# Kernel optimization log

Measured on AMD Instinct MI355X. Metric: run time of the kernel, lower is better.

The kernel has to match this reference:

```python
import jax, jax.numpy as jnp
import numpy as np

B, N, C_IN, C_OUT = 2, 163842, 64, 64  # icosphere level-7 vertex count
K = 7  # 1-ring neighborhood size (center + 6 neighbors)


def setup_inputs() -> dict:
    key = jax.random.key(0)
    kx, kw, kb, kn = jax.random.split(key, 4)
    x = jax.random.normal(kx, (B, N, C_IN), dtype=jnp.float32)
    # nn.Linear(7*in_feats, out_feats): W is (out, 7*in), bias (out,)
    W = jax.random.normal(kw, (C_OUT, K * C_IN), dtype=jnp.float32) * (1.0 / np.sqrt(K * C_IN))
    b = jax.random.normal(kb, (C_OUT,), dtype=jnp.float32) * 0.01
    neigh_orders = jax.random.randint(kn, (K * N,), 0, N, dtype=jnp.int64)
    return {"x": x, "W": W, "b": b, "neigh_orders": neigh_orders}


def reference(x, W, b, neigh_orders):
    # Faithful translation of onering_conv_layer_batch.forward:
    #   x: (B, N, C) -> permute -> (B, C, N)
    #   gather 7N indices on vertex axis -> (B, C, 7N)
    #   view -> (B, N, 7C)  (raw reshape of the (C, 7N) block, as in the torch code)
    #   Linear(7C -> out)
    Bb, Nn, Cc = x.shape
    xp = jnp.transpose(x, (0, 2, 1))            # (B, C, N)
    g = jnp.take(xp, neigh_orders, axis=2)      # (B, C, 7N)
    mat = g.reshape(Bb, Nn, K * Cc)             # (B, N, 7C)
    return jnp.einsum('bnk,ok->bno', mat, W) + b
```

## Files before the change

### kernel.cpp

```cpp
#include <hip/hip_runtime.h>

typedef short bf8_t __attribute__((ext_vector_type(8)));
typedef float f32x4 __attribute__((ext_vector_type(4)));

static constexpr int Bc      = 2;
static constexpr int Nv      = 163842;
static constexpr int CIN     = 64;
static constexpr int COUT    = 64;
static constexpr int KK      = 448;
static constexpr int SEVEN_N = 7 * Nv;
static constexpr int Q       = 3;
static constexpr int LM      = Q * KK;
static constexpr int MSTAGE  = LM + KK;
static constexpr int STRIDE  = 1800;
static constexpr int NT      = (SEVEN_N + LM - 1) / LM;
static constexpr int THREADS = 512;

__device__ inline unsigned pack2_bf16(float a, float b) {
    unsigned ua = __builtin_bit_cast(unsigned, a);
    unsigned ub = __builtin_bit_cast(unsigned, b);
    ua = (ua + 0x7FFFu + ((ua >> 16) & 1u)) >> 16;
    ub = (ub + 0x7FFFu + ((ub >> 16) & 1u));
    return (ua & 0xFFFFu) | (ub & 0xFFFF0000u);
}

__global__ __launch_bounds__(256) void xconv(const float* __restrict__ x,
                                             short* __restrict__ xb, int n) {
    const int i = (blockIdx.x * 256 + threadIdx.x) * 8;
    if (i >= n) return;
    const float4 a = *(const float4*)(x + i);
    const float4 c = *(const float4*)(x + i + 4);
    uint4 o;
    o.x = pack2_bf16(a.x, a.y); o.y = pack2_bf16(a.z, a.w);
    o.z = pack2_bf16(c.x, c.y); o.w = pack2_bf16(c.z, c.w);
    *(uint4*)(xb + i) = o;
}

__global__ __launch_bounds__(THREADS, 4) void conv_main_bf16(
    const short* __restrict__ xbf,
    const short* __restrict__ Wb,
    const float* __restrict__ bias,
    const int*   __restrict__ idx,
    float*       __restrict__ out)
{
    __shared__ short tile[16 * STRIDE];

    const int bid   = blockIdx.x;
    const int s     = bid & 7;
    const int b     = s & 1;
    const int mtres = s >> 1;
    const int rr    = bid >> 3;
    const int mt    = (rr >> 2) * 4 + mtres;
    const int cg    = rr & 3;
    if (mt >= NT) return;

    const int t    = threadIdx.x;
    const int M0   = mt * LM;
    const int mEnd = min(M0 + MSTAGE, SEVEN_N);
    const short* xb = xbf + (size_t)b * Nv * CIN;

    const int q     = t & 1;
    const int mloc  = t >> 1;
    const int choff = cg * 16 + q * 8;

    int iv[7];
    #pragma unroll
    for (int p = 0; p < 7; ++p) {
        const int m = M0 + p * 256 + mloc;
        iv[p] = (m < mEnd) ? idx[m] : 0;
    }
    bf8_t v[7];
    #pragma unroll
    for (int p = 0; p < 7; ++p)
        v[p] = *(const bf8_t*)(xb + (size_t)iv[p] * CIN + choff);
    #pragma unroll
    for (int p = 0; p < 7; ++p) {
        const int m = M0 + p * 256 + mloc;
        if (m < mEnd) {
            const int dm = m - M0;
            #pragma unroll
            for (int j = 0; j < 8; ++j) {
                const int c     = q * 8 + j;
                const int shift = (6 * c) & 7;
                tile[c * STRIDE + dm + shift] = v[p][j];
            }
        }
    }
    __syncthreads();

    const int lane = t & 63;
    const int w    = t >> 6;
    const int col  = lane & 15;
    const int hi   = lane >> 4;
    const int oc   = w & 3;

    const short* wbase = Wb + (oc * 16 + col) * KK + 8 * hi;
    bf8_t bfrag[14];
    #pragma unroll
    for (int k0 = 0; k0 < 14; ++k0)
        bfrag[k0] = *(const bf8_t*)(wbase + 32 * k0);

    const int Ca  = cg * 16 + col;
    const int Ta  = Ca * SEVEN_N + M0;
    const int d0a = (448 - (Ta % 448)) % 448;
    const int sha = Ta & 7;
    const short* abase0 = &tile[col * STRIDE + d0a + sha + 8 * hi];
    const float bo = bias[oc * 16 + col];

    for (int task = w; task < 12; task += 8) {
        const int r = task >> 2;
        const short* abase = abase0 + 448 * r;

        f32x4 acc = (f32x4){0.f, 0.f, 0.f, 0.f};
        #pragma unroll
        for (int k0 = 0; k0 < 14; ++k0) {
            const bf8_t afrag = *(const bf8_t*)(abase + 32 * k0);
            acc = __builtin_amdgcn_mfma_f32_16x16x32_bf16(afrag, bfrag[k0], acc, 0, 0, 0);
        }
        #pragma unroll
        for (int i = 0; i < 4; ++i) {
            const int c_s = 4 * hi + i;
            const int Cs  = cg * 16 + c_s;
            const int Ts  = Cs * SEVEN_N + M0;
            const int d0s = (448 - (Ts % 448)) % 448;
            const int sr  = M0 + d0s + 448 * r;
            if (sr + 448 <= SEVEN_N) {
                const int n = (Ts + d0s) / 448 + r;
                out[((size_t)b * Nv + n) * COUT + oc * 16 + col] = acc[i] + bo;
            }
        }
    }
}

static constexpr int PAIRS  = MSTAGE / 2;
static constexpr int PPP    = THREADS / 4;
static constexpr int PASSES = PAIRS / PPP;

__global__ __launch_bounds__(THREADS, 4) void conv_main_f32(
    const float* __restrict__ x,
    const short* __restrict__ Wb,
    const float* __restrict__ bias,
    const int*   __restrict__ idx,
    float*       __restrict__ out)
{
    __shared__ short tile[16 * STRIDE];

    const int bid  = blockIdx.x;
    const int slot = bid & 7;
    const int cg   = slot >> 1;
    const int b    = slot & 1;
    const int mt   = bid >> 3;
    const int t    = threadIdx.x;
    const int M0   = mt * LM;
    const int mEnd = min(M0 + MSTAGE, SEVEN_N);
    const float* xb = x + (size_t)b * Nv * CIN;

    const int q    = t & 3;
    const int pidl = t >> 2;
    const int xoff = cg * 16 + q * 4;

    int iv0[PASSES], iv1[PASSES];
    #pragma unroll
    for (int p = 0; p < PASSES; ++p) {
        const int m0 = M0 + 2 * (p * PPP + pidl);
        const bool ok = (m0 < mEnd);
        iv0[p] = ok ? idx[m0] : 0;
        iv1[p] = (ok && m0 + 1 < mEnd) ? idx[m0 + 1] : 0;
    }
    float4 v0[PASSES], v1[PASSES];
    #pragma unroll
    for (int p = 0; p < PASSES; ++p) {
        v0[p] = *(const float4*)(xb + (size_t)iv0[p] * CIN + xoff);
        v1[p] = *(const float4*)(xb + (size_t)iv1[p] * CIN + xoff);
    }
    #pragma unroll
    for (int p = 0; p < PASSES; ++p) {
        const int m0 = M0 + 2 * (p * PPP + pidl);
        if (m0 < mEnd) {
            const float a0[4] = {v0[p].x, v0[p].y, v0[p].z, v0[p].w};
            const float a1[4] = {v1[p].x, v1[p].y, v1[p].z, v1[p].w};
            #pragma unroll
            for (int i = 0; i < 4; ++i) {
                const int c     = q * 4 + i;
                const int shift = (6 * c) & 7;
                const int ppos  = (m0 - M0) + shift;
                *(unsigned*)&tile[c * STRIDE + ppos] = pack2_bf16(a0[i], a1[i]);
            }
        }
    }
    __syncthreads();

    const int lane = t & 63;
    const int w    = t >> 6;
    const int col  = lane & 15;
    const int hi   = lane >> 4;
    const int oc   = w & 3;

    const short* wbase = Wb + (oc * 16 + col) * KK + 8 * hi;
    bf8_t bfrag[14];
    #pragma unroll
    for (int k0 = 0; k0 < 14; ++k0)
        bfrag[k0] = *(const bf8_t*)(wbase + 32 * k0);

    const int Ca  = cg * 16 + col;
    const int Ta  = Ca * SEVEN_N + M0;
    const int d0a = (448 - (Ta % 448)) % 448;
    const int sha = Ta & 7;
    const short* abase0 = &tile[col * STRIDE + d0a + sha + 8 * hi];
    const float bo = bias[oc * 16 + col];

    for (int task = w; task < 12; task += 8) {
        const int r = task >> 2;
        const short* abase = abase0 + 448 * r;
        f32x4 acc = (f32x4){0.f, 0.f, 0.f, 0.f};
        #pragma unroll
        for (int k0 = 0; k0 < 14; ++k0) {
            const bf8_t afrag = *(const bf8_t*)(abase + 32 * k0);
            acc = __builtin_amdgcn_mfma_f32_16x16x32_bf16(afrag, bfrag[k0], acc, 0, 0, 0);
        }
        #pragma unroll
        for (int i = 0; i < 4; ++i) {
            const int c_s = 4 * hi + i;
            const int Cs  = cg * 16 + c_s;
            const int Ts  = Cs * SEVEN_N + M0;
            const int d0s = (448 - (Ts % 448)) % 448;
            const int sr  = M0 + d0s + 448 * r;
            if (sr + 448 <= SEVEN_N) {
                const int n = (Ts + d0s) / 448 + r;
                out[((size_t)b * Nv + n) * COUT + oc * 16 + col] = acc[i] + bo;
            }
        }
    }
}

__global__ __launch_bounds__(256) void conv_cleanup(
    const float* __restrict__ x,
    const float* __restrict__ W,
    const float* __restrict__ bias,
    const int*   __restrict__ idx,
    float*       __restrict__ out)
{
    __shared__ float part[4][64];
    const int C = blockIdx.x;
    const int b = blockIdx.y;
    const int t = threadIdx.x;
    const int o = t & 63;
    const int p = t >> 6;
    const int n = (int)(((long long)(C + 1) * SEVEN_N + 447) / 448) - 1;
    const int s = 448 * n - C * SEVEN_N;
    if (s + 448 <= SEVEN_N) return;
    const float* xb = x + (size_t)b * Nv * CIN;
    float acc = 0.f;
    for (int j = p * 112; j < (p + 1) * 112; ++j) {
        int m = s + j, c = C;
        if (m >= SEVEN_N) { m -= SEVEN_N; c += 1; }
        acc += xb[(size_t)idx[m] * CIN + c] * W[o * KK + j];
    }
    part[p][o] = acc;
    __syncthreads();
    if (p == 0)
        out[((size_t)b * Nv + n) * COUT + o] =
            part[0][o] + part[1][o] + part[2][o] + part[3][o] + bias[o];
}

__global__ void wconv(const float* __restrict__ W, short* __restrict__ Wb) {
    const int i = blockIdx.x * 256 + threadIdx.x;
    if (i < COUT * KK) {
        unsigned u = __builtin_bit_cast(unsigned, W[i]);
        u = (u + 0x7FFFu + ((u >> 16) & 1u)) >> 16;
        Wb[i] = (short)u;
    }
}

extern "C" void kernel_launch(void* const* d_in, const int* in_sizes, int n_in,
                              void* d_out, int out_size, void* d_ws, size_t ws_size,
                              hipStream_t stream) {
    const float* x    = (const float*)d_in[0];
    const float* W    = (const float*)d_in[1];
    const float* bias = (const float*)d_in[2];
    const int*   idx  = (const int*)d_in[3];
    float*       out  = (float*)d_out;
    short*       Wb   = (short*)d_ws;

    hipLaunchKernelGGL(wconv, dim3((COUT * KK + 255) / 256), dim3(256), 0, stream, W, Wb);

    const int    nxe    = Bc * Nv * CIN;
    const size_t need   = 65536 + (size_t)nxe * sizeof(short);
    if (ws_size >= need) {
        short* xbf = (short*)((char*)d_ws + 65536);
        hipLaunchKernelGGL(xconv, dim3((nxe / 8 + 255) / 256), dim3(256), 0, stream,
                           x, xbf, nxe);
        hipLaunchKernelGGL(conv_main_bf16, dim3(856 * 8), dim3(THREADS), 0, stream,
                           xbf, Wb, bias, idx, out);
    } else {
        hipLaunchKernelGGL(conv_main_f32, dim3(NT * 8), dim3(THREADS), 0, stream,
                           x, Wb, bias, idx, out);
    }
    hipLaunchKernelGGL(conv_cleanup, dim3(CIN, Bc), dim3(256), 0, stream,
                       x, W, bias, idx, out);
}
```

Measured before the change: 216.3 us.

## Shrink bf16 conv tile to two row-blocks per block for higher occupancy

Each block in the bf16 path now covers 2 output row-blocks instead of 3, so every wave runs exactly one MFMA task and the task loop is gone. The smaller LDS tile, with a new stride and a padding offset per 8-channel half, lets launch bounds rise from 4 to 6 blocks per CU. The grid grows to match. The cost is more redundant halo gathering, since each block still loads one extra 448-element overlap and that overlap is now larger relative to the useful work.

```diff
diff --git a/kernel.cpp b/kernel.cpp
--- a/kernel.cpp
+++ b/kernel.cpp
@@ -9,12 +9,17 @@
 static constexpr int COUT    = 64;
 static constexpr int KK      = 448;
 static constexpr int SEVEN_N = 7 * Nv;
-static constexpr int Q       = 3;
-static constexpr int LM      = Q * KK;
-static constexpr int MSTAGE  = LM + KK;
-static constexpr int STRIDE  = 1800;
-static constexpr int NT      = (SEVEN_N + LM - 1) / LM;
 static constexpr int THREADS = 512;
+
+static constexpr int LM2     = 2 * KK;
+static constexpr int MST2    = LM2 + KK;
+static constexpr int STRIDE2 = 1352;
+static constexpr int NT2     = (SEVEN_N + LM2 - 1) / LM2;
+static constexpr int TILE2   = 15 * STRIDE2 + 8 + STRIDE2;
+
+__device__ inline int cbase(int c) {
+    return c * STRIDE2 + 8 * (c >> 3);
+}
 
 __device__ inline unsigned pack2_bf16(float a, float b) {
     unsigned ua = __builtin_bit_cast(unsigned, a);
@@ -36,14 +41,14 @@
     *(uint4*)(xb + i) = o;
 }
 
-__global__ __launch_bounds__(THREADS, 4) void conv_main_bf16(
+__global__ __launch_bounds__(THREADS, 6) void conv_main_bf16(
     const short* __restrict__ xbf,
     const short* __restrict__ Wb,
     const float* __restrict__ bias,
     const int*   __restrict__ idx,
     float*       __restrict__ out)
 {
-    __shared__ short tile[16 * STRIDE];
+    __shared__ short tile[TILE2];
 
     const int bid   = blockIdx.x;
     const int s     = bid & 7;
@@ -52,37 +57,38 @@
     const int rr    = bid >> 3;
     const int mt    = (rr >> 2) * 4 + mtres;
     const int cg    = rr & 3;
-    if (mt >= NT) return;
+    if (mt >= NT2) return;
 
     const int t    = threadIdx.x;
-    const int M0   = mt * LM;
-    const int mEnd = min(M0 + MSTAGE, SEVEN_N);
+    const int M0   = mt * LM2;
+    const int mEnd = min(M0 + MST2, SEVEN_N);
     const short* xb = xbf + (size_t)b * Nv * CIN;
 
     const int q     = t & 1;
     const int mloc  = t >> 1;
     const int choff = cg * 16 + q * 8;
 
-    int iv[7];
-    #pragma unroll
-    for (int p = 0; p < 7; ++p) {
-        const int m = M0 + p * 256 + mloc;
-        iv[p] = (m < mEnd) ? idx[m] : 0;
-    }
-    bf8_t v[7];
-    #pragma unroll
-    for (int p = 0; p < 7; ++p)
+    int iv[6];
+    #pragma unroll
+    for (int p = 0; p < 6; ++p) {
+        const int dm = p * 256 + mloc;
+        const int m  = M0 + dm;
+        iv[p] = (dm < MST2 && m < mEnd) ? idx[m] : 0;
+    }
+    bf8_t v[6];
+    #pragma unroll
+    for (int p = 0; p < 6; ++p)
         v[p] = *(const bf8_t*)(xb + (size_t)iv[p] * CIN + choff);
     #pragma unroll
-    for (int p = 0; p < 7; ++p) {
-        const int m = M0 + p * 256 + mloc;
-        if (m < mEnd) {
-            const int dm = m - M0;
+    for (int p = 0; p < 6; ++p) {
+        const int dm = p * 256 + mloc;
+        const int m  = M0 + dm;
+        if (dm < MST2 && m < mEnd) {
             #pragma unroll
             for (int j = 0; j < 8; ++j) {
                 const int c     = q * 8 + j;
                 const int shift = (6 * c) & 7;
-                tile[c * STRIDE + dm + shift] = v[p][j];
+                tile[cbase(c) + dm + shift] = v[p][j];
             }
         }
     }
@@ -93,6 +99,7 @@
     const int col  = lane & 15;
     const int hi   = lane >> 4;
     const int oc   = w & 3;
+    const int r    = w >> 2;
 
     const short* wbase = Wb + (oc * 16 + col) * KK + 8 * hi;
     bf8_t bfrag[14];
@@ -104,37 +111,38 @@
     const int Ta  = Ca * SEVEN_N + M0;
     const int d0a = (448 - (Ta % 448)) % 448;
     const int sha = Ta & 7;
-    const short* abase0 = &tile[col * STRIDE + d0a + sha + 8 * hi];
+    const short* abase = &tile[cbase(col) + d0a + sha + 8 * hi + 448 * r];
+
+    f32x4 acc = (f32x4){0.f, 0.f, 0.f, 0.f};
+    #pragma unroll
+    for (int k0 = 0; k0 < 14; ++k0) {
+        const bf8_t afrag = *(const bf8_t*)(abase + 32 * k0);
+        acc = __builtin_amdgcn_mfma_f32_16x16x32_bf16(afrag, bfrag[k0], acc, 0, 0, 0);
+    }
+
     const float bo = bias[oc * 16 + col];
-
-    for (int task = w; task < 12; task += 8) {
-        const int r = task >> 2;
-        const short* abase = abase0 + 448 * r;
-
-        f32x4 acc = (f32x4){0.f, 0.f, 0.f, 0.f};
-        #pragma unroll
-        for (int k0 = 0; k0 < 14; ++k0) {
-            const bf8_t afrag = *(const bf8_t*)(abase + 32 * k0);
-            acc = __builtin_amdgcn_mfma_f32_16x16x32_bf16(afrag, bfrag[k0], acc, 0, 0, 0);
-        }
-        #pragma unroll
-        for (int i = 0; i < 4; ++i) {
-            const int c_s = 4 * hi + i;
-            const int Cs  = cg * 16 + c_s;
-            const int Ts  = Cs * SEVEN_N + M0;
-            const int d0s = (448 - (Ts % 448)) % 448;
-            const int sr  = M0 + d0s + 448 * r;
-            if (sr + 448 <= SEVEN_N) {
-                const int n = (Ts + d0s) / 448 + r;
-                out[((size_t)b * Nv + n) * COUT + oc * 16 + col] = acc[i] + bo;
-            }
-        }
-    }
-}
-
-static constexpr int PAIRS  = MSTAGE / 2;
-static constexpr int PPP    = THREADS / 4;
-static constexpr int PASSES = PAIRS / PPP;
+    #pragma unroll
+    for (int i = 0; i < 4; ++i) {
+        const int c_s = 4 * hi + i;
+        const int Cs  = cg * 16 + c_s;
+        const int Ts  = Cs * SEVEN_N + M0;
+        const int d0s = (448 - (Ts % 448)) % 448;
+        const int sr  = M0 + d0s + 448 * r;
+        if (sr + 448 <= SEVEN_N) {
+            const int n = (Ts + d0s) / 448 + r;
+            out[((size_t)b * Nv + n) * COUT + oc * 16 + col] = acc[i] + bo;
+        }
+    }
+}
+
+static constexpr int Q3      = 3;
+static constexpr int LM3     = Q3 * KK;
+static constexpr int MST3    = LM3 + KK;
+static constexpr int STRIDE3 = 1800;
+static constexpr int NT3     = (SEVEN_N + LM3 - 1) / LM3;
+static constexpr int PAIRS   = MST3 / 2;
+static constexpr int PPP     = THREADS / 4;
+static constexpr int PASSES  = PAIRS / PPP;
 
 __global__ __launch_bounds__(THREADS, 4) void conv_main_f32(
     const float* __restrict__ x,
@@ -143,7 +151,7 @@
     const int*   __restrict__ idx,
     float*       __restrict__ out)
 {
-    __shared__ short tile[16 * STRIDE];
+    __shared__ short tile[16 * STRIDE3];
 
     const int bid  = blockIdx.x;
     const int slot = bid & 7;
@@ -151,8 +159,8 @@
     const int b    = slot & 1;
     const int mt   = bid >> 3;
     const int t    = threadIdx.x;
-    const int M0   = mt * LM;
-    const int mEnd = min(M0 + MSTAGE, SEVEN_N);
+    const int M0   = mt * LM3;
+    const int mEnd = min(M0 + MST3, SEVEN_N);
     const float* xb = x + (size_t)b * Nv * CIN;
 
     const int q    = t & 3;
@@ -184,7 +192,7 @@
                 const int c     = q * 4 + i;
                 const int shift = (6 * c) & 7;
                 const int ppos  = (m0 - M0) + shift;
-                *(unsigned*)&tile[c * STRIDE + ppos] = pack2_bf16(a0[i], a1[i]);
+                *(unsigned*)&tile[c * STRIDE3 + ppos] = pack2_bf16(a0[i], a1[i]);
             }
         }
     }
@@ -206,7 +214,7 @@
     const int Ta  = Ca * SEVEN_N + M0;
     const int d0a = (448 - (Ta % 448)) % 448;
     const int sha = Ta & 7;
-    const short* abase0 = &tile[col * STRIDE + d0a + sha + 8 * hi];
+    const short* abase0 = &tile[col * STRIDE3 + d0a + sha + 8 * hi];
     const float bo = bias[oc * 16 + col];
 
     for (int task = w; task < 12; task += 8) {
@@ -284,16 +292,16 @@
 
     hipLaunchKernelGGL(wconv, dim3((COUT * KK + 255) / 256), dim3(256), 0, stream, W, Wb);
 
-    const int    nxe    = Bc * Nv * CIN;
-    const size_t need   = 65536 + (size_t)nxe * sizeof(short);
+    const int    nxe  = Bc * Nv * CIN;
+    const size_t need = 65536 + (size_t)nxe * sizeof(short);
     if (ws_size >= need) {
         short* xbf = (short*)((char*)d_ws + 65536);
         hipLaunchKernelGGL(xconv, dim3((nxe / 8 + 255) / 256), dim3(256), 0, stream,
                            x, xbf, nxe);
-        hipLaunchKernelGGL(conv_main_bf16, dim3(856 * 8), dim3(THREADS), 0, stream,
+        hipLaunchKernelGGL(conv_main_bf16, dim3(321 * 4 * 8), dim3(THREADS), 0, stream,
                            xbf, Wb, bias, idx, out);
     } else {
-        hipLaunchKernelGGL(conv_main_f32, dim3(NT * 8), dim3(THREADS), 0, stream,
+        hipLaunchKernelGGL(conv_main_f32, dim3(NT3 * 8), dim3(THREADS), 0, stream,
                            x, Wb, bias, idx, out);
     }
     hipLaunchKernelGGL(conv_cleanup, dim3(CIN, Bc), dim3(256), 0, stream,
```

Measured after the change: 242.3 us. +12.0%, slower.
